# Kernel optimization log

Hardware: AMD Instinct MI355X
Metric: run time of the kernel (lower is better)

The kernel has to match this reference:

```python
import jax, jax.numpy as jnp
import numpy as np

N_NODES = 4096
N_SUBS = 1024
NUM_FEATURES = 128
HIDDEN = 512
NHEADS = 8
DHEAD = HIDDEN // NHEADS
NUM_LAYERS = 2
EDGE_PROB = 0.01
NEG_INF = -1e9


def _make_adj(key, n, p):
    a = (jax.random.uniform(key, (n, n)) < p).astype(jnp.float32)
    return jnp.maximum(a, jnp.eye(n, dtype=jnp.float32))  # self-loops


def setup_inputs() -> dict:
    key = jax.random.key(0)
    ks = jax.random.split(key, 12)
    x = jax.random.normal(ks[0], (N_NODES, NUM_FEATURES), dtype=jnp.float32)
    adj_node = _make_adj(ks[1], N_NODES, EDGE_PROB)
    adj_substation = _make_adj(ks[2], N_SUBS, 4 * EDGE_PROB)
    seg_ids = jnp.sort(jax.random.randint(ks[3], (N_NODES,), 0, N_SUBS, dtype=jnp.int32))
    s = 0.05
    lin_w = jax.random.normal(ks[4], (NUM_FEATURES, HIDDEN), dtype=jnp.float32) * s
    lin_b = jnp.zeros((HIDDEN,), dtype=jnp.float32)
    node_W = jax.random.normal(ks[5], (NUM_LAYERS, HIDDEN, HIDDEN), dtype=jnp.float32) * s
    node_asrc = jax.random.normal(ks[6], (NUM_LAYERS, NHEADS, DHEAD), dtype=jnp.float32) * s
    node_adst = jax.random.normal(ks[7], (NUM_LAYERS, NHEADS, DHEAD), dtype=jnp.float32) * s
    sub_W = jax.random.normal(ks[8], (NUM_LAYERS, HIDDEN, HIDDEN), dtype=jnp.float32) * s
    sub_asrc = jax.random.normal(ks[9], (NUM_LAYERS, NHEADS, DHEAD), dtype=jnp.float32) * s
    sub_adst = jax.random.normal(ks[10], (NUM_LAYERS, NHEADS, DHEAD), dtype=jnp.float32) * s
    return {"x": x, "adj_node": adj_node, "adj_substation": adj_substation,
            "seg_ids": seg_ids, "lin_w": lin_w, "lin_b": lin_b,
            "node_W": node_W, "node_asrc": node_asrc, "node_adst": node_adst,
            "sub_W": sub_W, "sub_asrc": sub_asrc, "sub_adst": sub_adst}


def _gat_layer(h, adj, W, a_src, a_dst):
    # h: [N, F]; adj: [N, N]; W: [F, F]; a_src/a_dst: [H, Dh]
    n = h.shape[0]
    Wh = (h @ W).reshape(n, NHEADS, DHEAD)               # [N, H, Dh]
    f_src = jnp.einsum('nhd,hd->hn', Wh, a_src)          # [H, N]
    f_dst = jnp.einsum('nhd,hd->hn', Wh, a_dst)          # [H, N]
    e = jax.nn.leaky_relu(f_src[:, :, None] + f_dst[:, None, :], 0.2)  # [H, N, N]
    e = jnp.where(adj[None] > 0, e, NEG_INF)
    alpha = jax.nn.softmax(e, axis=-1)                   # [H, N, N]
    out = jnp.einsum('hij,jhd->ihd', alpha, Wh).reshape(n, NHEADS * DHEAD)
    return jax.nn.elu(out)


def _stacked_gats(h, adj, Ws, asrcs, adsts):
    # Faithful to the source bug: x is never rebound, each layer sees the
    # original input; the last layer's output is returned.
    out = h
    for i in range(Ws.shape[0]):
        out = _gat_layer(h, adj, Ws[i], asrcs[i], adsts[i])
    return out


def _pool_mean(h, seg_ids, num_segments):
    sums = jax.ops.segment_sum(h, seg_ids, num_segments=num_segments)
    counts = jax.ops.segment_sum(jnp.ones((h.shape[0], 1), h.dtype), seg_ids,
                                 num_segments=num_segments)
    return sums / jnp.maximum(counts, 1.0)


def reference(x, adj_node, adj_substation, seg_ids, lin_w, lin_b,
              node_W, node_asrc, node_adst, sub_W, sub_asrc, sub_adst):
    h = x @ lin_w + lin_b                                  # [N, HIDDEN]
    h = _stacked_gats(h, adj_node, node_W, node_asrc, node_adst)
    s = _pool_mean(h, seg_ids, N_SUBS)                     # [S, HIDDEN]
    s = _stacked_gats(s, adj_substation, sub_W, sub_asrc, sub_adst)
    return s
```

## Files before the change

kernel.cpp:

```cpp
#include <hip/hip_runtime.h>
#include <hip/hip_bf16.h>
#include <hip/hip_fp16.h>
#include <math.h>

#define N_NODES 4096
#define N_SUBS  1024
#define NFEAT   128
#define HIDDEN  512
#define NHEADS  8
#define DHEAD   64
#define CAP     128
#define ROWG    4
#define HGS     8

typedef float vfloat4 __attribute__((ext_vector_type(4)));

struct alignas(16) h8 { __half2 a, b, c, d; };

__global__ __launch_bounds__(256) void extract_both(const float* __restrict__ adj_n,
                                                    const float* __restrict__ adj_s,
                                                    int* __restrict__ cnt_n,
                                                    int* __restrict__ nbr_n,
                                                    int* __restrict__ cnt_s,
                                                    int* __restrict__ nbr_s) {
    const int w = threadIdx.x >> 6;
    const int lane = threadIdx.x & 63;
    const float* adj;
    int N, row;
    int* cnt;
    int* nbr;
    if (blockIdx.x < N_NODES / 4) {
        adj = adj_n; N = N_NODES; cnt = cnt_n; nbr = nbr_n;
        row = blockIdx.x * 4 + w;
    } else {
        adj = adj_s; N = N_SUBS; cnt = cnt_s; nbr = nbr_s;
        row = (blockIdx.x - N_NODES / 4) * 4 + w;
    }
    const vfloat4* rowp = (const vfloat4*)(adj + (size_t)row * N);
    int* nrow = nbr + (row << 7);
    const int n4 = N >> 2;
    int c = 0;
    const unsigned long long below = (1ull << lane) - 1ull;
    for (int c4 = lane; c4 < n4; c4 += 64) {
        const vfloat4 v = __builtin_nontemporal_load(&rowp[c4]);
        const int col = c4 << 2;
        unsigned long long m;
        bool p;
        p = v.x > 0.0f; m = __ballot(p);
        if (p) { int q = c + __popcll(m & below); if (q < CAP) nrow[q] = col; }
        c += __popcll(m);
        p = v.y > 0.0f; m = __ballot(p);
        if (p) { int q = c + __popcll(m & below); if (q < CAP) nrow[q] = col + 1; }
        c += __popcll(m);
        p = v.z > 0.0f; m = __ballot(p);
        if (p) { int q = c + __popcll(m & below); if (q < CAP) nrow[q] = col + 2; }
        c += __popcll(m);
        p = v.w > 0.0f; m = __ballot(p);
        if (p) { int q = c + __popcll(m & below); if (q < CAP) nrow[q] = col + 3; }
        c += __popcll(m);
    }
    if (lane == 0) cnt[row] = c < CAP ? c : CAP;
}

#define BM 64
#define BN 64
#define BK 16
__global__ __launch_bounds__(256) void gemm_f32(const float* __restrict__ A,
                                                const float* __restrict__ B,
                                                const float* __restrict__ bias,
                                                float* __restrict__ C,
                                                int M, int N, int K, int k_chunk,
                                                const float* __restrict__ asrc,
                                                const float* __restrict__ adst,
                                                float* __restrict__ fs,
                                                float* __restrict__ fd,
                                                const float* __restrict__ lin_b,
                                                float* __restrict__ bias_part,
                                                __half* __restrict__ C_h) {
    __shared__ float As[BK][BM + 4];
    __shared__ float Bs[BK][BN + 4];
    const int tid = threadIdx.x;
    const int bm = blockIdx.y * BM;
    const int bn = blockIdx.x * BN;
    const int k_start = blockIdx.z * k_chunk;
    const int k_end = (k_start + k_chunk) < K ? (k_start + k_chunk) : K;
    if (lin_b && blockIdx.y == gridDim.y - 1) {
        const int q = tid >> 6;
        const int n = tid & 63;
        const int sub = k_chunk >> 2;
        const int kb = k_start + q * sub;
        float s = 0.0f;
        for (int k = 0; k < sub; k++)
            s += lin_b[kb + k] * B[(size_t)(kb + k) * N + bn + n];
        float* red = (float*)As;
        red[q * 64 + n] = s;
        __syncthreads();
        if (q == 0) {
            s = red[n] + red[64 + n] + red[128 + n] + red[192 + n];
            bias_part[blockIdx.z * N + bn + n] = s;
        }
        return;
    }
    float* Cw = C + (size_t)blockIdx.z * M * N;
    const int tr = tid >> 4;
    const int tc = tid & 15;
    const int am = tid >> 2;
    const int ak4 = (tid & 3) * 4;
    const int bk = tid >> 4;
    const int bn0 = (tid & 15) * 4;
    float acc[4][4] = {};
    for (int k0 = k_start; k0 < k_end; k0 += BK) {
        const float4 va = *(const float4*)&A[(size_t)(bm + am) * K + k0 + ak4];
        const float4 vb = *(const float4*)&B[(size_t)(k0 + bk) * N + bn + bn0];
        As[ak4 + 0][am] = va.x;
        As[ak4 + 1][am] = va.y;
        As[ak4 + 2][am] = va.z;
        As[ak4 + 3][am] = va.w;
        *(float4*)&Bs[bk][bn0] = vb;
        __syncthreads();
#pragma unroll
        for (int k = 0; k < BK; k++) {
            const float4 a4 = *(const float4*)&As[k][tr * 4];
            const float4 b4 = *(const float4*)&Bs[k][tc * 4];
            const float a[4] = {a4.x, a4.y, a4.z, a4.w};
            const float b[4] = {b4.x, b4.y, b4.z, b4.w};
#pragma unroll
            for (int i = 0; i < 4; i++)
#pragma unroll
                for (int j = 0; j < 4; j++)
                    acc[i][j] += a[i] * b[j];
        }
        __syncthreads();
    }
#pragma unroll
    for (int i = 0; i < 4; i++) {
        const int m = bm + tr * 4 + i;
        if (bias) {
            const float4 bv = *(const float4*)&bias[bn + tc * 4];
            acc[i][0] += bv.x; acc[i][1] += bv.y; acc[i][2] += bv.z; acc[i][3] += bv.w;
        }
        if (C_h) {
            __half2 p0 = __floats2half2_rn(acc[i][0], acc[i][1]);
            __half2 p1 = __floats2half2_rn(acc[i][2], acc[i][3]);
            __half2* hp = (__half2*)&C_h[(size_t)m * N + bn + tc * 4];
            hp[0] = p0;
            hp[1] = p1;
        } else {
            float4 o = {acc[i][0], acc[i][1], acc[i][2], acc[i][3]};
            *(float4*)&Cw[(size_t)m * N + bn + tc * 4] = o;
        }
    }
    if (asrc) {
        const int h = blockIdx.x;
        const float4 as4 = *(const float4*)&asrc[h * DHEAD + tc * 4];
        const float4 ad4 = *(const float4*)&adst[h * DHEAD + tc * 4];
#pragma unroll
        for (int i = 0; i < 4; i++) {
            float vs = acc[i][0] * as4.x + acc[i][1] * as4.y +
                       acc[i][2] * as4.z + acc[i][3] * as4.w;
            float vd = acc[i][0] * ad4.x + acc[i][1] * ad4.y +
                       acc[i][2] * ad4.z + acc[i][3] * ad4.w;
#pragma unroll
            for (int off = 1; off < 16; off <<= 1) {
                vs += __shfl_xor(vs, off, 64);
                vd += __shfl_xor(vd, off, 64);
            }
            if (tc == 0) {
                const int m = bm + tr * 4 + i;
                fs[h * M + m] = vs;
                fd[h * M + m] = vd;
            }
        }
    }
}

__global__ __launch_bounds__(256) void reduce_both(const float* __restrict__ p1,
                                                   float* __restrict__ o1,
                                                   int len1, int nz1,
                                                   const float* __restrict__ p2,
                                                   float* __restrict__ o2,
                                                   int len2, int nz2,
                                                   int blocks1) {
    if ((int)blockIdx.x < blocks1) {
        const int i = blockIdx.x * 256 + threadIdx.x;
        if (i < len1) {
            float s = 0.0f;
            for (int z = 0; z < nz1; z++) s += p1[(size_t)z * len1 + i];
            o1[i] = s;
        }
    } else {
        const int i = (blockIdx.x - blocks1) * 256 + threadIdx.x;
        if (i < len2) {
            float s = 0.0f;
            for (int z = 0; z < nz2; z++) s += p2[(size_t)z * len2 + i];
            o2[i] = s;
        }
    }
}

__global__ __launch_bounds__(512) void reduce_fsfd(const float* __restrict__ part,
                                                   float* __restrict__ wh,
                                                   const float* __restrict__ asrc,
                                                   const float* __restrict__ adst,
                                                   float* __restrict__ fs,
                                                   float* __restrict__ fd,
                                                   int M, int nz) {
    const int n = blockIdx.x;
    const int tid = threadIdx.x;
    float v = 0.0f;
    for (int z = 0; z < nz; z++)
        v += part[((size_t)z * M + n) * HIDDEN + tid];
    wh[(size_t)n * HIDDEN + tid] = v;
    const int h = tid >> 6;
    const int d = tid & 63;
    float vs = v * asrc[h * DHEAD + d];
    float vd = v * adst[h * DHEAD + d];
#pragma unroll
    for (int off = 32; off >= 1; off >>= 1) {
        vs += __shfl_xor(vs, off, 64);
        vd += __shfl_xor(vd, off, 64);
    }
    if (d == 0) {
        fs[h * M + n] = vs;
        fd[h * M + n] = vd;
    }
}

__device__ __forceinline__ void gat_softmax(const float* __restrict__ fs,
                                            const float* __restrict__ fd,
                                            const int* snbr, float (*ex)[CAP + 1],
                                            int C, int i, int N, int tid) {
    const int h = tid >> 6;
    const int lane = tid & 63;
    const float fsi = fs[h * N + i];
    const float* __restrict__ fdh = fd + h * N;
    float m = -1e30f;
    for (int k = lane; k < C; k += 64) {
        float e = fsi + fdh[snbr[k]];
        e = e > 0.0f ? e : 0.2f * e;
        ex[h][k] = e;
        m = fmaxf(m, e);
    }
#pragma unroll
    for (int off = 32; off >= 1; off >>= 1) m = fmaxf(m, __shfl_xor(m, off, 64));
    float ssum = 0.0f;
    for (int k = lane; k < C; k += 64) {
        float v = __expf(ex[h][k] - m);
        ex[h][k] = v;
        ssum += v;
    }
#pragma unroll
    for (int off = 32; off >= 1; off >>= 1) ssum += __shfl_xor(ssum, off, 64);
    const float inv = 1.0f / ssum;
    for (int k = lane; k < C; k += 64) ex[h][k] *= inv;
}

__global__ __launch_bounds__(512) void gat_agg_h(const __half* __restrict__ Wh,
                                                 const float* __restrict__ fs,
                                                 const float* __restrict__ fd,
                                                 const int* __restrict__ cnt,
                                                 const int* __restrict__ nbr,
                                                 float* __restrict__ out, int N) {
    __shared__ int snbr[CAP];
    __shared__ float ex[NHEADS][CAP + 1];
    __shared__ float sacc[HGS][HIDDEN];
    const int i = blockIdx.x;
    const int tid = threadIdx.x;
    int C = cnt[i];
    C = C < CAP ? C : CAP;
    for (int k = tid; k < C; k += 512) snbr[k] = nbr[(i << 7) + k];
    __syncthreads();
    gat_softmax(fs, fd, snbr, ex, C, i, N, tid);
    __syncthreads();
    const int g = tid >> 6;
    const int t = tid & 63;
    const int hh = t >> 3;
    float a0f[8] = {};
    float* acc = a0f;
    int k = g;
    for (; k + 3 * HGS < C; k += 4 * HGS) {
        const int j0 = snbr[k];
        const int j1 = snbr[k + HGS];
        const int j2 = snbr[k + 2 * HGS];
        const int j3 = snbr[k + 3 * HGS];
        const float a0 = ex[hh][k];
        const float a1 = ex[hh][k + HGS];
        const float a2 = ex[hh][k + 2 * HGS];
        const float a3 = ex[hh][k + 3 * HGS];
        const h8 w0 = *(const h8*)&Wh[(size_t)j0 * HIDDEN + 8 * t];
        const h8 w1 = *(const h8*)&Wh[(size_t)j1 * HIDDEN + 8 * t];
        const h8 w2 = *(const h8*)&Wh[(size_t)j2 * HIDDEN + 8 * t];
        const h8 w3 = *(const h8*)&Wh[(size_t)j3 * HIDDEN + 8 * t];
        float2 f;
        f = __half22float2(w0.a); acc[0] += a0 * f.x; acc[1] += a0 * f.y;
        f = __half22float2(w0.b); acc[2] += a0 * f.x; acc[3] += a0 * f.y;
        f = __half22float2(w0.c); acc[4] += a0 * f.x; acc[5] += a0 * f.y;
        f = __half22float2(w0.d); acc[6] += a0 * f.x; acc[7] += a0 * f.y;
        f = __half22float2(w1.a); acc[0] += a1 * f.x; acc[1] += a1 * f.y;
        f = __half22float2(w1.b); acc[2] += a1 * f.x; acc[3] += a1 * f.y;
        f = __half22float2(w1.c); acc[4] += a1 * f.x; acc[5] += a1 * f.y;
        f = __half22float2(w1.d); acc[6] += a1 * f.x; acc[7] += a1 * f.y;
        f = __half22float2(w2.a); acc[0] += a2 * f.x; acc[1] += a2 * f.y;
        f = __half22float2(w2.b); acc[2] += a2 * f.x; acc[3] += a2 * f.y;
        f = __half22float2(w2.c); acc[4] += a2 * f.x; acc[5] += a2 * f.y;
        f = __half22float2(w2.d); acc[6] += a2 * f.x; acc[7] += a2 * f.y;
        f = __half22float2(w3.a); acc[0] += a3 * f.x; acc[1] += a3 * f.y;
        f = __half22float2(w3.b); acc[2] += a3 * f.x; acc[3] += a3 * f.y;
        f = __half22float2(w3.c); acc[4] += a3 * f.x; acc[5] += a3 * f.y;
        f = __half22float2(w3.d); acc[6] += a3 * f.x; acc[7] += a3 * f.y;
    }
    for (; k < C; k += HGS) {
        const int j0 = snbr[k];
        const float a0 = ex[hh][k];
        const h8 w0 = *(const h8*)&Wh[(size_t)j0 * HIDDEN + 8 * t];
        float2 f;
        f = __half22float2(w0.a); acc[0] += a0 * f.x; acc[1] += a0 * f.y;
        f = __half22float2(w0.b); acc[2] += a0 * f.x; acc[3] += a0 * f.y;
        f = __half22float2(w0.c); acc[4] += a0 * f.x; acc[5] += a0 * f.y;
        f = __half22float2(w0.d); acc[6] += a0 * f.x; acc[7] += a0 * f.y;
    }
    *(float4*)&sacc[g][8 * t] = *(float4*)&acc[0];
    *(float4*)&sacc[g][8 * t + 4] = *(float4*)&acc[4];
    __syncthreads();
    if (g == 0) {
#pragma unroll
        for (int e = 0; e < 8; e++) {
            float r = acc[e];
#pragma unroll
            for (int gg = 1; gg < HGS; gg++) r += sacc[gg][8 * t + e];
            out[(size_t)i * HIDDEN + 8 * t + e] =
                r > 0.0f ? r : __expf(r) - 1.0f;
        }
    }
}

__global__ __launch_bounds__(512) void gat_agg_f(const float* __restrict__ Wh,
                                                 const float* __restrict__ fs,
                                                 const float* __restrict__ fd,
                                                 const int* __restrict__ cnt,
                                                 const int* __restrict__ nbr,
                                                 float* __restrict__ out, int N) {
    __shared__ int snbr[CAP];
    __shared__ float ex[NHEADS][CAP + 1];
    __shared__ float sacc[ROWG][HIDDEN];
    const int i = blockIdx.x;
    const int tid = threadIdx.x;
    int C = cnt[i];
    C = C < CAP ? C : CAP;
    for (int k = tid; k < C; k += 512) snbr[k] = nbr[(i << 7) + k];
    __syncthreads();
    gat_softmax(fs, fd, snbr, ex, C, i, N, tid);
    __syncthreads();
    const int g = tid >> 7;
    const int t = tid & 127;
    const int hh = t >> 4;
    float4 acc = {0.f, 0.f, 0.f, 0.f};
    int k = g;
    for (; k + 3 * ROWG < C; k += 4 * ROWG) {
        const int j0 = snbr[k];
        const int j1 = snbr[k + ROWG];
        const int j2 = snbr[k + 2 * ROWG];
        const int j3 = snbr[k + 3 * ROWG];
        const float a0 = ex[hh][k];
        const float a1 = ex[hh][k + ROWG];
        const float a2 = ex[hh][k + 2 * ROWG];
        const float a3 = ex[hh][k + 3 * ROWG];
        const float4 w0 = *(const float4*)&Wh[(size_t)j0 * HIDDEN + 4 * t];
        const float4 w1 = *(const float4*)&Wh[(size_t)j1 * HIDDEN + 4 * t];
        const float4 w2 = *(const float4*)&Wh[(size_t)j2 * HIDDEN + 4 * t];
        const float4 w3 = *(const float4*)&Wh[(size_t)j3 * HIDDEN + 4 * t];
        acc.x += a0 * w0.x + a1 * w1.x + a2 * w2.x + a3 * w3.x;
        acc.y += a0 * w0.y + a1 * w1.y + a2 * w2.y + a3 * w3.y;
        acc.z += a0 * w0.z + a1 * w1.z + a2 * w2.z + a3 * w3.z;
        acc.w += a0 * w0.w + a1 * w1.w + a2 * w2.w + a3 * w3.w;
    }
    for (; k < C; k += ROWG) {
        const int j0 = snbr[k];
        const float a0 = ex[hh][k];
        const float4 w0 = *(const float4*)&Wh[(size_t)j0 * HIDDEN + 4 * t];
        acc.x += a0 * w0.x; acc.y += a0 * w0.y;
        acc.z += a0 * w0.z; acc.w += a0 * w0.w;
    }
    *(float4*)&sacc[g][4 * t] = acc;
    __syncthreads();
    if (g == 0) {
        float4 r = acc;
#pragma unroll
        for (int gg = 1; gg < ROWG; gg++) {
            const float4 o = *(const float4*)&sacc[gg][4 * t];
            r.x += o.x; r.y += o.y; r.z += o.z; r.w += o.w;
        }
        r.x = r.x > 0.0f ? r.x : __expf(r.x) - 1.0f;
        r.y = r.y > 0.0f ? r.y : __expf(r.y) - 1.0f;
        r.z = r.z > 0.0f ? r.z : __expf(r.z) - 1.0f;
        r.w = r.w > 0.0f ? r.w : __expf(r.w) - 1.0f;
        *(float4*)&out[(size_t)i * HIDDEN + 4 * t] = r;
    }
}

__global__ __launch_bounds__(512) void pool_kernel(const float* __restrict__ hin,
                                                   const int* __restrict__ seg,
                                                   float* __restrict__ sout) {
    const int s = blockIdx.x;
    const int d = threadIdx.x;
    int lo = 0, hi = N_NODES;
    while (lo < hi) { int mid = (lo + hi) >> 1; if (seg[mid] < s) lo = mid + 1; else hi = mid; }
    const int start = lo;
    hi = N_NODES;
    while (lo < hi) { int mid = (lo + hi) >> 1; if (seg[mid] < s + 1) lo = mid + 1; else hi = mid; }
    const int end = lo;
    float acc = 0.0f;
    for (int r = start; r < end; r++) acc += hin[(size_t)r * HIDDEN + d];
    const int c = end - start;
    sout[(size_t)s * HIDDEN + d] = acc / (c > 0 ? (float)c : 1.0f);
}

extern "C" void kernel_launch(void* const* d_in, const int* in_sizes, int n_in,
                              void* d_out, int out_size, void* d_ws, size_t ws_size,
                              hipStream_t stream) {
    const float* x        = (const float*)d_in[0];
    const float* adj_node = (const float*)d_in[1];
    const float* adj_sub  = (const float*)d_in[2];
    const int*   seg_ids  = (const int*)d_in[3];
    const float* lin_w    = (const float*)d_in[4];
    const float* lin_b    = (const float*)d_in[5];
    const float* node_W1    = (const float*)d_in[6]  + HIDDEN * HIDDEN;
    const float* node_asrc1 = (const float*)d_in[7]  + NHEADS * DHEAD;
    const float* node_adst1 = (const float*)d_in[8]  + NHEADS * DHEAD;
    const float* sub_W1     = (const float*)d_in[9]  + HIDDEN * HIDDEN;
    const float* sub_asrc1  = (const float*)d_in[10] + NHEADS * DHEAD;
    const float* sub_adst1  = (const float*)d_in[11] + NHEADS * DHEAD;
    float* out = (float*)d_out;

    char* ws = (char*)d_ws;
    float* bufA  = (float*)(ws);
    float* bufB  = (float*)(ws + (size_t)8 * 1024 * 1024);
    float* fs_n  = (float*)(ws + (size_t)16 * 1024 * 1024);
    float* fd_n  = fs_n + NHEADS * N_NODES;
    float* fs_s  = fd_n + NHEADS * N_NODES;
    float* fd_s  = fs_s + NHEADS * N_SUBS;
    int*   cnt_n = (int*)(fd_s + NHEADS * N_SUBS);
    int*   cnt_s = cnt_n + N_NODES;
    int*   nbr_n = cnt_s + N_SUBS;
    int*   nbr_s = nbr_n + N_NODES * CAP;

    float*  Wpart = bufB;
    float*  Wfuse = bufB + 16 * NFEAT * HIDDEN;
    float*  bpart = Wfuse + NFEAT * HIDDEN;
    float*  bias2 = bpart + 16 * HIDDEN;
    __half* wh_n  = (__half*)bufA;
    float*  gatom = bufB;
    float*  sp    = bufA;
    float*  Spart = bufB;
    float*  wh_s  = bufA + (size_t)N_SUBS * HIDDEN;

    extract_both<<<N_NODES / 4 + N_SUBS / 4, 256, 0, stream>>>(
        adj_node, adj_sub, cnt_n, nbr_n, cnt_s, nbr_s);
    gemm_f32<<<dim3(HIDDEN / BN, NFEAT / BM + 1, 16), 256, 0, stream>>>(
        lin_w, node_W1, nullptr, Wpart, NFEAT, HIDDEN, HIDDEN, HIDDEN / 16,
        nullptr, nullptr, nullptr, nullptr, lin_b, bpart, nullptr);
    reduce_both<<<NFEAT * HIDDEN / 256 + 2, 256, 0, stream>>>(
        Wpart, Wfuse, NFEAT * HIDDEN, 16, bpart, bias2, HIDDEN, 16,
        NFEAT * HIDDEN / 256);
    gemm_f32<<<dim3(HIDDEN / BN, N_NODES / BM, 1), 256, 0, stream>>>(
        x, Wfuse, bias2, nullptr, N_NODES, HIDDEN, NFEAT, NFEAT,
        node_asrc1, node_adst1, fs_n, fd_n, nullptr, nullptr, wh_n);
    gat_agg_h<<<N_NODES, 512, 0, stream>>>(wh_n, fs_n, fd_n, cnt_n, nbr_n,
                                           gatom, N_NODES);
    pool_kernel<<<N_SUBS, 512, 0, stream>>>(gatom, seg_ids, sp);
    gemm_f32<<<dim3(HIDDEN / BN, N_SUBS / BM, 4), 256, 0, stream>>>(
        sp, sub_W1, nullptr, Spart, N_SUBS, HIDDEN, HIDDEN, HIDDEN / 4,
        nullptr, nullptr, nullptr, nullptr, nullptr, nullptr, nullptr);
    reduce_fsfd<<<N_SUBS, 512, 0, stream>>>(Spart, wh_s, sub_asrc1, sub_adst1,
                                            fs_s, fd_s, N_SUBS, 4);
    gat_agg_f<<<N_SUBS, 512, 0, stream>>>(wh_s, fs_s, fd_s, cnt_s, nbr_s,
                                          out, N_SUBS);
}
```

Before: 208.9 us.

## Merge extract, weight-fold GEMM and pool zeroing; fuse mean pooling into aggregation

Result: slower. 241.1 us (+15.4%).

```diff
diff --git a/kernel.cpp b/kernel.cpp
--- a/kernel.cpp
+++ b/kernel.cpp
@@ -17,54 +17,141 @@
 
 struct alignas(16) h8 { __half2 a, b, c, d; };
 
-__global__ __launch_bounds__(256) void extract_both(const float* __restrict__ adj_n,
-                                                    const float* __restrict__ adj_s,
-                                                    int* __restrict__ cnt_n,
-                                                    int* __restrict__ nbr_n,
-                                                    int* __restrict__ cnt_s,
-                                                    int* __restrict__ nbr_s) {
-    const int w = threadIdx.x >> 6;
-    const int lane = threadIdx.x & 63;
-    const float* adj;
-    int N, row;
-    int* cnt;
-    int* nbr;
-    if (blockIdx.x < N_NODES / 4) {
-        adj = adj_n; N = N_NODES; cnt = cnt_n; nbr = nbr_n;
-        row = blockIdx.x * 4 + w;
-    } else {
-        adj = adj_s; N = N_SUBS; cnt = cnt_s; nbr = nbr_s;
-        row = (blockIdx.x - N_NODES / 4) * 4 + w;
-    }
-    const vfloat4* rowp = (const vfloat4*)(adj + (size_t)row * N);
-    int* nrow = nbr + (row << 7);
-    const int n4 = N >> 2;
-    int c = 0;
-    const unsigned long long below = (1ull << lane) - 1ull;
-    for (int c4 = lane; c4 < n4; c4 += 64) {
-        const vfloat4 v = __builtin_nontemporal_load(&rowp[c4]);
-        const int col = c4 << 2;
-        unsigned long long m;
-        bool p;
-        p = v.x > 0.0f; m = __ballot(p);
-        if (p) { int q = c + __popcll(m & below); if (q < CAP) nrow[q] = col; }
-        c += __popcll(m);
-        p = v.y > 0.0f; m = __ballot(p);
-        if (p) { int q = c + __popcll(m & below); if (q < CAP) nrow[q] = col + 1; }
-        c += __popcll(m);
-        p = v.z > 0.0f; m = __ballot(p);
-        if (p) { int q = c + __popcll(m & below); if (q < CAP) nrow[q] = col + 2; }
-        c += __popcll(m);
-        p = v.w > 0.0f; m = __ballot(p);
-        if (p) { int q = c + __popcll(m & below); if (q < CAP) nrow[q] = col + 3; }
-        c += __popcll(m);
-    }
-    if (lane == 0) cnt[row] = c < CAP ? c : CAP;
-}
-
+#define NB_EXTRACT (N_NODES / 4 + N_SUBS / 4)
+#define NB_GEMM    (8 * 3 * 16)
+#define NB_ZERO    128
 #define BM 64
 #define BN 64
 #define BK 16
+
+__global__ __launch_bounds__(256) void phase1(const float* __restrict__ adj_n,
+                                              const float* __restrict__ adj_s,
+                                              int* __restrict__ cnt_n,
+                                              int* __restrict__ nbr_n,
+                                              int* __restrict__ cnt_s,
+                                              int* __restrict__ nbr_s,
+                                              const float* __restrict__ lin_w,
+                                              const float* __restrict__ node_W1,
+                                              const float* __restrict__ lin_b,
+                                              float* __restrict__ Wpart,
+                                              float* __restrict__ bpart,
+                                              float* __restrict__ sp) {
+    const int tid = threadIdx.x;
+    if (blockIdx.x < NB_EXTRACT) {
+        const int w = tid >> 6;
+        const int lane = tid & 63;
+        const float* adj;
+        int N, row;
+        int* cnt;
+        int* nbr;
+        if (blockIdx.x < N_NODES / 4) {
+            adj = adj_n; N = N_NODES; cnt = cnt_n; nbr = nbr_n;
+            row = blockIdx.x * 4 + w;
+        } else {
+            adj = adj_s; N = N_SUBS; cnt = cnt_s; nbr = nbr_s;
+            row = (blockIdx.x - N_NODES / 4) * 4 + w;
+        }
+        const vfloat4* rowp = (const vfloat4*)(adj + (size_t)row * N);
+        int* nrow = nbr + (row << 7);
+        const int n4 = N >> 2;
+        int c = 0;
+        const unsigned long long below = (1ull << lane) - 1ull;
+        for (int c4 = lane; c4 < n4; c4 += 64) {
+            const vfloat4 v = __builtin_nontemporal_load(&rowp[c4]);
+            const int col = c4 << 2;
+            unsigned long long m;
+            bool p;
+            p = v.x > 0.0f; m = __ballot(p);
+            if (p) { int q = c + __popcll(m & below); if (q < CAP) nrow[q] = col; }
+            c += __popcll(m);
+            p = v.y > 0.0f; m = __ballot(p);
+            if (p) { int q = c + __popcll(m & below); if (q < CAP) nrow[q] = col + 1; }
+            c += __popcll(m);
+            p = v.z > 0.0f; m = __ballot(p);
+            if (p) { int q = c + __popcll(m & below); if (q < CAP) nrow[q] = col + 2; }
+            c += __popcll(m);
+            p = v.w > 0.0f; m = __ballot(p);
+            if (p) { int q = c + __popcll(m & below); if (q < CAP) nrow[q] = col + 3; }
+            c += __popcll(m);
+        }
+        if (lane == 0) cnt[row] = c < CAP ? c : CAP;
+        return;
+    }
+    if (blockIdx.x < NB_EXTRACT + NB_GEMM) {
+        const int b = blockIdx.x - NB_EXTRACT;
+        const int bn = (b & 7) * BN;
+        const int rem = b >> 3;
+        const int by = rem % 3;
+        const int bz = rem / 3;
+        const int M = NFEAT, N = HIDDEN, K = HIDDEN;
+        const int k_chunk = K / 16;
+        const int k_start = bz * k_chunk;
+        __shared__ float As[BK][BM + 4];
+        __shared__ float Bs[BK][BN + 4];
+        if (by == 2) {
+            const int q = tid >> 6;
+            const int n = tid & 63;
+            const int sub = k_chunk >> 2;
+            const int kb = k_start + q * sub;
+            float s = 0.0f;
+            for (int k = 0; k < sub; k++)
+                s += lin_b[kb + k] * node_W1[(size_t)(kb + k) * N + bn + n];
+            float* red = (float*)As;
+            red[q * 64 + n] = s;
+            __syncthreads();
+            if (q == 0)
+                bpart[bz * N + bn + n] = red[n] + red[64 + n] + red[128 + n] + red[192 + n];
+            return;
+        }
+        const int bm = by * BM;
+        float* Cw = Wpart + (size_t)bz * M * N;
+        const int tr = tid >> 4;
+        const int tc = tid & 15;
+        const int am = tid >> 2;
+        const int ak4 = (tid & 3) * 4;
+        const int bk = tid >> 4;
+        const int bn0 = (tid & 15) * 4;
+        float acc[4][4] = {};
+        for (int k0 = k_start; k0 < k_start + k_chunk; k0 += BK) {
+            const float4 va = *(const float4*)&lin_w[(size_t)(bm + am) * K + k0 + ak4];
+            const float4 vb = *(const float4*)&node_W1[(size_t)(k0 + bk) * N + bn + bn0];
+            As[ak4 + 0][am] = va.x;
+            As[ak4 + 1][am] = va.y;
+            As[ak4 + 2][am] = va.z;
+            As[ak4 + 3][am] = va.w;
+            *(float4*)&Bs[bk][bn0] = vb;
+            __syncthreads();
+#pragma unroll
+            for (int k = 0; k < BK; k++) {
+                const float4 a4 = *(const float4*)&As[k][tr * 4];
+                const float4 b4 = *(const float4*)&Bs[k][tc * 4];
+                const float a[4] = {a4.x, a4.y, a4.z, a4.w};
+                const float bb[4] = {b4.x, b4.y, b4.z, b4.w};
+#pragma unroll
+                for (int i = 0; i < 4; i++)
+#pragma unroll
+                    for (int j = 0; j < 4; j++)
+                        acc[i][j] += a[i] * bb[j];
+            }
+            __syncthreads();
+        }
+#pragma unroll
+        for (int i = 0; i < 4; i++) {
+            const int m = bm + tr * 4 + i;
+            float4 o = {acc[i][0], acc[i][1], acc[i][2], acc[i][3]};
+            *(float4*)&Cw[(size_t)m * N + bn + tc * 4] = o;
+        }
+        return;
+    }
+    {
+        const int b = blockIdx.x - NB_EXTRACT - NB_GEMM;
+        float4 z4 = {0.f, 0.f, 0.f, 0.f};
+        const int total4 = N_SUBS * HIDDEN / 4;
+        for (int idx = b * 256 + tid; idx < total4; idx += NB_ZERO * 256)
+            ((float4*)sp)[idx] = z4;
+    }
+}
+
 __global__ __launch_bounds__(256) void gemm_f32(const float* __restrict__ A,
                                                 const float* __restrict__ B,
                                                 const float* __restrict__ bias,
@@ -74,8 +161,6 @@
                                                 const float* __restrict__ adst,
                                                 float* __restrict__ fs,
                                                 float* __restrict__ fd,
-                                                const float* __restrict__ lin_b,
-                                                float* __restrict__ bias_part,
                                                 __half* __restrict__ C_h) {
     __shared__ float As[BK][BM + 4];
     __shared__ float Bs[BK][BN + 4];
@@ -84,23 +169,6 @@
     const int bn = blockIdx.x * BN;
     const int k_start = blockIdx.z * k_chunk;
     const int k_end = (k_start + k_chunk) < K ? (k_start + k_chunk) : K;
-    if (lin_b && blockIdx.y == gridDim.y - 1) {
-        const int q = tid >> 6;
-        const int n = tid & 63;
-        const int sub = k_chunk >> 2;
-        const int kb = k_start + q * sub;
-        float s = 0.0f;
-        for (int k = 0; k < sub; k++)
-            s += lin_b[kb + k] * B[(size_t)(kb + k) * N + bn + n];
-        float* red = (float*)As;
-        red[q * 64 + n] = s;
-        __syncthreads();
-        if (q == 0) {
-            s = red[n] + red[64 + n] + red[128 + n] + red[192 + n];
-            bias_part[blockIdx.z * N + bn + n] = s;
-        }
-        return;
-    }
     float* Cw = C + (size_t)blockIdx.z * M * N;
     const int tr = tid >> 4;
     const int tc = tid & 15;
@@ -260,7 +328,8 @@
                                                  const float* __restrict__ fd,
                                                  const int* __restrict__ cnt,
                                                  const int* __restrict__ nbr,
-                                                 float* __restrict__ out, int N) {
+                                                 const int* __restrict__ seg_ids,
+                                                 float* __restrict__ sp, int N) {
     __shared__ int snbr[CAP];
     __shared__ float ex[NHEADS][CAP + 1];
     __shared__ float sacc[HGS][HIDDEN];
@@ -323,13 +392,21 @@
     *(float4*)&sacc[g][8 * t + 4] = *(float4*)&acc[4];
     __syncthreads();
     if (g == 0) {
+        const int seg = seg_ids[i];
+        int lo = 0, hi = N_NODES;
+        while (lo < hi) { int mid = (lo + hi) >> 1; if (seg_ids[mid] < seg) lo = mid + 1; else hi = mid; }
+        const int start = lo;
+        hi = N_NODES;
+        while (lo < hi) { int mid = (lo + hi) >> 1; if (seg_ids[mid] < seg + 1) lo = mid + 1; else hi = mid; }
+        const float invc = 1.0f / (float)(lo - start);
+        float* dst = sp + (size_t)seg * HIDDEN + 8 * t;
 #pragma unroll
         for (int e = 0; e < 8; e++) {
             float r = acc[e];
 #pragma unroll
             for (int gg = 1; gg < HGS; gg++) r += sacc[gg][8 * t + e];
-            out[(size_t)i * HIDDEN + 8 * t + e] =
-                r > 0.0f ? r : __expf(r) - 1.0f;
+            r = r > 0.0f ? r : __expf(r) - 1.0f;
+            atomicAdd(dst + e, r * invc);
         }
     }
 }
@@ -398,23 +475,6 @@
     }
 }
 
-__global__ __launch_bounds__(512) void pool_kernel(const float* __restrict__ hin,
-                                                   const int* __restrict__ seg,
-                                                   float* __restrict__ sout) {
-    const int s = blockIdx.x;
-    const int d = threadIdx.x;
-    int lo = 0, hi = N_NODES;
-    while (lo < hi) { int mid = (lo + hi) >> 1; if (seg[mid] < s) lo = mid + 1; else hi = mid; }
-    const int start = lo;
-    hi = N_NODES;
-    while (lo < hi) { int mid = (lo + hi) >> 1; if (seg[mid] < s + 1) lo = mid + 1; else hi = mid; }
-    const int end = lo;
-    float acc = 0.0f;
-    for (int r = start; r < end; r++) acc += hin[(size_t)r * HIDDEN + d];
-    const int c = end - start;
-    sout[(size_t)s * HIDDEN + d] = acc / (c > 0 ? (float)c : 1.0f);
-}
-
 extern "C" void kernel_launch(void* const* d_in, const int* in_sizes, int n_in,
                               void* d_out, int out_size, void* d_ws, size_t ws_size,
                               hipStream_t stream) {
@@ -443,34 +503,30 @@
     int*   cnt_s = cnt_n + N_NODES;
     int*   nbr_n = cnt_s + N_SUBS;
     int*   nbr_s = nbr_n + N_NODES * CAP;
+    float* sp    = (float*)(nbr_s + N_SUBS * CAP);
 
     float*  Wpart = bufB;
     float*  Wfuse = bufB + 16 * NFEAT * HIDDEN;
     float*  bpart = Wfuse + NFEAT * HIDDEN;
     float*  bias2 = bpart + 16 * HIDDEN;
+    float*  Spart = bufB;
     __half* wh_n  = (__half*)bufA;
-    float*  gatom = bufB;
-    float*  sp    = bufA;
-    float*  Spart = bufB;
-    float*  wh_s  = bufA + (size_t)N_SUBS * HIDDEN;
-
-    extract_both<<<N_NODES / 4 + N_SUBS / 4, 256, 0, stream>>>(
-        adj_node, adj_sub, cnt_n, nbr_n, cnt_s, nbr_s);
-    gemm_f32<<<dim3(HIDDEN / BN, NFEAT / BM + 1, 16), 256, 0, stream>>>(
-        lin_w, node_W1, nullptr, Wpart, NFEAT, HIDDEN, HIDDEN, HIDDEN / 16,
-        nullptr, nullptr, nullptr, nullptr, lin_b, bpart, nullptr);
+    float*  wh_s  = bufA + (size_t)N_NODES * HIDDEN / 2;
+
+    phase1<<<NB_EXTRACT + NB_GEMM + NB_ZERO, 256, 0, stream>>>(
+        adj_node, adj_sub, cnt_n, nbr_n, cnt_s, nbr_s,
+        lin_w, node_W1, lin_b, Wpart, bpart, sp);
     reduce_both<<<NFEAT * HIDDEN / 256 + 2, 256, 0, stream>>>(
         Wpart, Wfuse, NFEAT * HIDDEN, 16, bpart, bias2, HIDDEN, 16,
         NFEAT * HIDDEN / 256);
     gemm_f32<<<dim3(HIDDEN / BN, N_NODES / BM, 1), 256, 0, stream>>>(
         x, Wfuse, bias2, nullptr, N_NODES, HIDDEN, NFEAT, NFEAT,
-        node_asrc1, node_adst1, fs_n, fd_n, nullptr, nullptr, wh_n);
+        node_asrc1, node_adst1, fs_n, fd_n, wh_n);
     gat_agg_h<<<N_NODES, 512, 0, stream>>>(wh_n, fs_n, fd_n, cnt_n, nbr_n,
-                                           gatom, N_NODES);
-    pool_kernel<<<N_SUBS, 512, 0, stream>>>(gatom, seg_ids, sp);
+                                           seg_ids, sp, N_NODES);
     gemm_f32<<<dim3(HIDDEN / BN, N_SUBS / BM, 4), 256, 0, stream>>>(
         sp, sub_W1, nullptr, Spart, N_SUBS, HIDDEN, HIDDEN, HIDDEN / 4,
-        nullptr, nullptr, nullptr, nullptr, nullptr, nullptr, nullptr);
+        nullptr, nullptr, nullptr, nullptr, nullptr);
     reduce_fsfd<<<N_SUBS, 512, 0, stream>>>(Spart, wh_s, sub_asrc1, sub_adst1,
                                             fs_s, fd_s, N_SUBS, 4);
     gat_agg_f<<<N_SUBS, 512, 0, stream>>>(wh_s, fs_s, fd_s, cnt_s, nbr_s,
```
